# Optimization experiments

Measured on AMD Instinct MI355X. Metric: run time of the kernel, lower is better.

## Reference

```python
import jax, jax.numpy as jnp
import numpy as np

B, S, E, H = 2, 2048, 1024, 16
HD = E // H  # head_dim = 64
NEG = jnp.float32(-1e9)


def setup_inputs() -> dict:
    key = jax.random.key(0)
    k1, k2, k3 = jax.random.split(key, 3)
    x = jax.random.normal(k1, (B, S, E), dtype=jnp.float32)
    w_qkv = jax.random.normal(k2, (E, 3 * E), dtype=jnp.float32) * 0.02
    b_qkv = jnp.zeros((3 * E,), dtype=jnp.float32)
    w_proj = jax.random.normal(k3, (E, E), dtype=jnp.float32) * 0.02
    b_proj = jnp.zeros((E,), dtype=jnp.float32)
    return {"x": x, "w_qkv": w_qkv, "b_qkv": b_qkv, "w_proj": w_proj, "b_proj": b_proj}


def reference(x, w_qkv, b_qkv, w_proj, b_proj):
    # c_attn (GPT2 Conv1D): x @ W + b -> [B,S,3E]
    qkv = x @ w_qkv + b_qkv
    q, k, v = jnp.split(qkv, 3, axis=-1)
    # split heads -> [B,H,S,HD]
    def heads(t):
        return t.reshape(B, S, H, HD).transpose(0, 2, 1, 3)
    q, k, v = heads(q), heads(k), heads(v)
    # scaled QK^T, causal mask, softmax (attn_pdrop=0 so dropout is identity)
    scores = jnp.einsum("bhqd,bhkd->bhqk", q, k) / jnp.sqrt(jnp.float32(HD))
    causal = jnp.tril(jnp.ones((S, S), dtype=bool))
    scores = jnp.where(causal, scores, NEG)
    attn = jax.nn.softmax(scores, axis=-1)
    out = jnp.einsum("bhqk,bhkd->bhqd", attn, v)
    out = out.transpose(0, 2, 1, 3).reshape(B, S, E)
    # c_proj
    return out @ w_proj + b_proj
```

## Files before the change

kernel.cpp:

```cpp
#include <hip/hip_runtime.h>


typedef __bf16 bf16;
typedef __bf16 bf16x4 __attribute__((ext_vector_type(4)));
typedef __bf16 bf16x8 __attribute__((ext_vector_type(8)));
typedef float f32x4 __attribute__((ext_vector_type(4)));

#define GLOBAL_AS(p) ((const __attribute__((address_space(1))) void*)(p))
#define LDS_AS(p) ((__attribute__((address_space(3))) void*)(p))

__device__ __forceinline__ void g2l16(const void* g, void* l) {
  __builtin_amdgcn_global_load_lds(GLOBAL_AS(g), LDS_AS(l), 16, 0, 0);
}

#define QSCL 0.18033688f

__global__ __launch_bounds__(256) void prep_kernel(
    const float* __restrict__ x, const float* __restrict__ wq,
    const float* __restrict__ wp, bf16* __restrict__ Xbf,
    bf16* __restrict__ Wqt, bf16* __restrict__ Wpt) {
  __shared__ float tile[32][33];
  const int t = threadIdx.x;
  const int b = blockIdx.x;
  if (b < 4096) {
    const int i = (b * 256 + t) * 4;
    const float4 v = *(const float4*)(x + i);
    bf16x4 o;
    o.x = (bf16)v.x; o.y = (bf16)v.y; o.z = (bf16)v.z; o.w = (bf16)v.w;
    *(bf16x4*)(Xbf + i) = o;
    return;
  }
  const float* W; bf16* Wt; int C, bx, by;
  if (b < 7168) {
    const int b2 = b - 4096;
    W = wq; Wt = Wqt; C = 3072; bx = b2 % 96; by = b2 / 96;
  } else {
    const int b3 = b - 7168;
    W = wp; Wt = Wpt; C = 1024; bx = b3 & 31; by = b3 >> 5;
  }
  const int c0 = bx * 32, r0 = by * 32;
  const int tx = t & 31, ty = t >> 5;
#pragma unroll
  for (int i = ty; i < 32; i += 8) tile[i][tx] = W[(r0 + i) * C + c0 + tx];
  __syncthreads();
#pragma unroll
  for (int i = ty; i < 32; i += 8)
    Wt[(c0 + i) * 1024 + r0 + tx] = (bf16)tile[tx][i];
}

__global__ __launch_bounds__(256) void gemm_qkv_kernel(
    const bf16* __restrict__ A, const bf16* __restrict__ Bt,
    const float* __restrict__ bias, bf16* __restrict__ Qo,
    bf16* __restrict__ Ko, bf16* __restrict__ Vto) {
  constexpr int K = 1024;
  __shared__ bf16 As[128 * 32];
  __shared__ bf16 Bs[128 * 32];
  const int t = threadIdx.x;
  const int m0 = blockIdx.x * 128;
  const int n0 = blockIdx.y * 128;
  const int wave = t >> 6, lane = t & 63;
  const int wr = (wave >> 1) * 64, wc = (wave & 1) * 64;
  const int lr = lane & 15, lg = lane >> 4;
  f32x4 acc[4][4] = {};
  const bf16* ag = A + (m0 + (t >> 2)) * K + (t & 3) * 8;
  const bf16* bg = Bt + (n0 + (t >> 2)) * K + (t & 3) * 8;
  for (int k0 = 0; k0 < K; k0 += 32) {
    __syncthreads();
    g2l16(ag, &As[t * 8]);
    g2l16(ag + 64 * K, &As[2048 + t * 8]);
    g2l16(bg, &Bs[t * 8]);
    g2l16(bg + 64 * K, &Bs[2048 + t * 8]);
    ag += 32; bg += 32;
    __syncthreads();
    bf16x8 af[4], bfr[4];
#pragma unroll
    for (int i = 0; i < 4; i++)
      af[i] = *(const bf16x8*)&As[(wr + i * 16 + lr) * 32 + lg * 8];
#pragma unroll
    for (int j = 0; j < 4; j++)
      bfr[j] = *(const bf16x8*)&Bs[(wc + j * 16 + lr) * 32 + lg * 8];
#pragma unroll
    for (int i = 0; i < 4; i++)
#pragma unroll
      for (int j = 0; j < 4; j++)
        acc[i][j] = __builtin_amdgcn_mfma_f32_16x16x32_bf16(af[i], bfr[j],
                                                            acc[i][j], 0, 0, 0);
  }
#pragma unroll
  for (int i = 0; i < 4; i++) {
#pragma unroll
    for (int j = 0; j < 4; j++) {
      const int n = n0 + wc + j * 16 + lr;
      const float bv = bias[n];
      if (n0 >= 2048) {
        const int e = n & 1023, h = e >> 6, d = e & 63;
        const int mb = m0 + wr + i * 16 + lg * 4;
        const int b = mb >> 11, s = mb & 2047;
        bf16x4 vv;
#pragma unroll
        for (int r = 0; r < 4; r++) vv[r] = (bf16)(acc[i][j][r] + bv);
        *(bf16x4*)(Vto + ((size_t)((b * 16 + h) * 64 + d)) * 2048 + s) = vv;
      } else {
        const int e = n & 1023, h = e >> 6, d = e & 63;
        const bool isq = (n < 1024);
        bf16* dst = isq ? Qo : Ko;
#pragma unroll
        for (int r = 0; r < 4; r++) {
          const int m = m0 + wr + i * 16 + lg * 4 + r;
          const int b = m >> 11, s = m & 2047;
          const float v = acc[i][j][r] + bv;
          dst[((b * 16 + h) * 2048 + s) * 64 + d] = (bf16)(isq ? v * QSCL : v);
        }
      }
    }
  }
}

__global__ __launch_bounds__(256) void gemm_proj_kernel(
    const bf16* __restrict__ A, const bf16* __restrict__ Bt,
    const float* __restrict__ bias, float* __restrict__ Cf) {
  constexpr int K = 1024, N = 1024;
  __shared__ bf16 As[64 * 32];
  __shared__ bf16 Bs[128 * 32];
  const int t = threadIdx.x;
  const int m0 = blockIdx.x * 64;
  const int n0 = blockIdx.y * 128;
  const int wave = t >> 6, lane = t & 63;
  const int wr = (wave >> 1) * 32, wc = (wave & 1) * 64;
  const int lr = lane & 15, lg = lane >> 4;
  f32x4 acc[2][4] = {};
  const bf16* ag = A + (m0 + (t >> 2)) * K + (t & 3) * 8;
  const bf16* bg = Bt + (n0 + (t >> 2)) * K + (t & 3) * 8;
  for (int k0 = 0; k0 < K; k0 += 32) {
    __syncthreads();
    g2l16(ag, &As[t * 8]);
    g2l16(bg, &Bs[t * 8]);
    g2l16(bg + 64 * K, &Bs[2048 + t * 8]);
    ag += 32; bg += 32;
    __syncthreads();
    bf16x8 af[2], bfr[4];
#pragma unroll
    for (int i = 0; i < 2; i++)
      af[i] = *(const bf16x8*)&As[(wr + i * 16 + lr) * 32 + lg * 8];
#pragma unroll
    for (int j = 0; j < 4; j++)
      bfr[j] = *(const bf16x8*)&Bs[(wc + j * 16 + lr) * 32 + lg * 8];
#pragma unroll
    for (int i = 0; i < 2; i++)
#pragma unroll
      for (int j = 0; j < 4; j++)
        acc[i][j] = __builtin_amdgcn_mfma_f32_16x16x32_bf16(af[i], bfr[j],
                                                            acc[i][j], 0, 0, 0);
  }
#pragma unroll
  for (int i = 0; i < 2; i++) {
#pragma unroll
    for (int j = 0; j < 4; j++) {
      const int n = n0 + wc + j * 16 + lr;
      const float bv = bias[n];
#pragma unroll
      for (int r = 0; r < 4; r++) {
        const int m = m0 + wr + i * 16 + lg * 4 + r;
        Cf[m * N + n] = acc[i][j][r] + bv;
      }
    }
  }
}

__device__ __forceinline__ void stage_kv(const bf16* __restrict__ Kg,
                                         const bf16* __restrict__ Vg, int kb,
                                         bf16* ks, bf16* vs, int t) {
  int u = t, r = u >> 3, c = (u & 7) ^ (r & 7);
  g2l16(Kg + (kb + r) * 64 + c * 8, ks + u * 8);
  g2l16(Vg + r * 2048 + kb + c * 8, vs + u * 8);
  u = 256 + t; r = u >> 3; c = (u & 7) ^ (r & 7);
  g2l16(Kg + (kb + r) * 64 + c * 8, ks + u * 8);
  g2l16(Vg + r * 2048 + kb + c * 8, vs + u * 8);
}

__global__ __launch_bounds__(256, 4) void attn_kernel(
    const bf16* __restrict__ Qb, const bf16* __restrict__ Kb,
    const bf16* __restrict__ Vt, bf16* __restrict__ Obf) {
  __shared__ bf16 Ks[64 * 64];
  __shared__ bf16 Vs[64 * 64];
  __shared__ bf16 Ps[4][16 * 72];
  const int t = threadIdx.x;
  const int w = t >> 6, lane = t & 63;
  const int lr = lane & 15, lg = lane >> 4;
  const int bx = blockIdx.x;
  const int xcd = bx & 7, idx = bx >> 3;
  const int bh = (idx & 3) * 8 + xcd;
  const int strip = 31 - (idx >> 2);
  const int qb = strip * 64 + w * 16;
  const bf16* Qg = Qb + (size_t)bh * 2048 * 64;
  const bf16* Kg = Kb + (size_t)bh * 2048 * 64;
  const bf16* Vg = Vt + (size_t)bh * 64 * 2048;
  bf16x8 bq[2];
#pragma unroll
  for (int h = 0; h < 2; h++)
    bq[h] = *(const bf16x8*)(Qg + (qb + lr) * 64 + h * 32 + lg * 8);
  f32x4 oacc[4] = {};
  float lsum = 0.f;
  bf16* ps = &Ps[w][0];
  const int T = strip + 1;
  for (int ti = 0; ti < T; ++ti) {
    __syncthreads();
    stage_kv(Kg, Vg, ti * 64, Ks, Vs, t);
    __syncthreads();
    const int kb = ti * 64;
    bf16x8 ak[4][2], av[4][2];
#pragma unroll
    for (int j = 0; j < 4; j++) {
      const int row = j * 16 + lr;
#pragma unroll
      for (int h = 0; h < 2; h++)
        ak[j][h] =
            *(const bf16x8*)(Ks + (row * 8 + ((h * 4 + lg) ^ (row & 7))) * 8);
    }
#pragma unroll
    for (int dt = 0; dt < 4; dt++) {
      const int row = dt * 16 + lr;
#pragma unroll
      for (int h = 0; h < 2; h++)
        av[dt][h] =
            *(const bf16x8*)(Vs + (row * 8 + ((h * 4 + lg) ^ (row & 7))) * 8);
    }
    f32x4 sacc[4];
#pragma unroll
    for (int j = 0; j < 4; j++) {
      f32x4 s = {};
      s = __builtin_amdgcn_mfma_f32_16x16x32_bf16(ak[j][0], bq[0], s, 0, 0, 0);
      s = __builtin_amdgcn_mfma_f32_16x16x32_bf16(ak[j][1], bq[1], s, 0, 0, 0);
      sacc[j] = s;
    }
    const bool diag = (kb + 63 > qb);
    bf16x4 pk[4];
#pragma unroll
    for (int j = 0; j < 4; j++)
#pragma unroll
      for (int r = 0; r < 4; r++) {
        float v = sacc[j][r];
        if (diag && (kb + j * 16 + lg * 4 + r > qb + lr)) v = -1e30f;
        const float e = __builtin_amdgcn_exp2f(v);
        lsum += e;
        pk[j][r] = (bf16)e;
      }
    asm volatile("" ::: "memory");
#pragma unroll
    for (int j = 0; j < 4; j++)
      *(bf16x4*)(ps + lr * 72 + j * 16 + lg * 4) = pk[j];
    asm volatile("s_waitcnt lgkmcnt(0)" ::: "memory");
    bf16x8 bp[2];
#pragma unroll
    for (int h = 0; h < 2; h++)
      bp[h] = *(const bf16x8*)(ps + lr * 72 + h * 32 + lg * 8);
#pragma unroll
    for (int dt = 0; dt < 4; dt++) {
      f32x4 o = oacc[dt];
      o = __builtin_amdgcn_mfma_f32_16x16x32_bf16(av[dt][0], bp[0], o, 0, 0, 0);
      o = __builtin_amdgcn_mfma_f32_16x16x32_bf16(av[dt][1], bp[1], o, 0, 0, 0);
      oacc[dt] = o;
    }
  }
  lsum += __shfl_xor(lsum, 16, 64);
  lsum += __shfl_xor(lsum, 32, 64);
  const float inv = 1.0f / lsum;
  const int b = bh >> 4, hh = bh & 15;
  const int q = qb + lr;
  bf16* orow = Obf + ((size_t)(b * 2048 + q)) * 1024 + hh * 64;
#pragma unroll
  for (int dt = 0; dt < 4; dt++) {
    bf16x4 ov;
#pragma unroll
    for (int r = 0; r < 4; r++) ov[r] = (bf16)(oacc[dt][r] * inv);
    *(bf16x4*)(orow + dt * 16 + lg * 4) = ov;
  }
}

extern "C" void kernel_launch(void* const* d_in, const int* in_sizes, int n_in,
                              void* d_out, int out_size, void* d_ws,
                              size_t ws_size, hipStream_t stream) {
  const float* x      = (const float*)d_in[0];
  const float* w_qkv  = (const float*)d_in[1];
  const float* b_qkv  = (const float*)d_in[2];
  const float* w_proj = (const float*)d_in[3];
  const float* b_proj = (const float*)d_in[4];
  float* out = (float*)d_out;

  char* w = (char*)d_ws;
  bf16* Xbf = (bf16*)w;  w += 4096 * 1024 * 2;
  bf16* Wqt = (bf16*)w;  w += 3072 * 1024 * 2;
  bf16* Wpt = (bf16*)w;  w += 1024 * 1024 * 2;
  bf16* Qb  = (bf16*)w;  w += 2 * 16 * 2048 * 64 * 2;
  bf16* Kb  = (bf16*)w;  w += 2 * 16 * 2048 * 64 * 2;
  bf16* Vt  = (bf16*)w;  w += 2 * 16 * 64 * 2048 * 2;
  bf16* Obf = (bf16*)w;  w += 4096 * 1024 * 2;

  prep_kernel<<<8192, 256, 0, stream>>>(x, w_qkv, w_proj, Xbf, Wqt, Wpt);
  gemm_qkv_kernel<<<dim3(32, 24), 256, 0, stream>>>(
      Xbf, Wqt, b_qkv, Qb, Kb, Vt);
  attn_kernel<<<1024, 256, 0, stream>>>(Qb, Kb, Vt, Obf);
  gemm_proj_kernel<<<dim3(64, 8), 256, 0, stream>>>(Obf, Wpt, b_proj, out);
}
```

Baseline: 170.1 us.

## Double K-step to 64 and XOR-swizzle LDS layout in QKV GEMM

The QKV projection GEMM now stages 64-wide K slices per iteration instead of 32, which halves the number of barrier pairs per block. Each 16-byte chunk's column index is XOR-swizzled by its row in LDS, and reads use the same swizzle, to avoid bank conflicts on the fragment loads. This doubles shared memory per block and increases register use for the fragments, which may reduce occupancy.

```diff
diff --git a/kernel.cpp b/kernel.cpp
--- a/kernel.cpp
+++ b/kernel.cpp
@@ -53,8 +53,8 @@
     const float* __restrict__ bias, bf16* __restrict__ Qo,
     bf16* __restrict__ Ko, bf16* __restrict__ Vto) {
   constexpr int K = 1024;
-  __shared__ bf16 As[128 * 32];
-  __shared__ bf16 Bs[128 * 32];
+  __shared__ bf16 As[128 * 64];
+  __shared__ bf16 Bs[128 * 64];
   const int t = threadIdx.x;
   const int m0 = blockIdx.x * 128;
   const int n0 = blockIdx.y * 128;
@@ -62,29 +62,41 @@
   const int wr = (wave >> 1) * 64, wc = (wave & 1) * 64;
   const int lr = lane & 15, lg = lane >> 4;
   f32x4 acc[4][4] = {};
-  const bf16* ag = A + (m0 + (t >> 2)) * K + (t & 3) * 8;
-  const bf16* bg = Bt + (n0 + (t >> 2)) * K + (t & 3) * 8;
-  for (int k0 = 0; k0 < K; k0 += 32) {
-    __syncthreads();
-    g2l16(ag, &As[t * 8]);
-    g2l16(ag + 64 * K, &As[2048 + t * 8]);
-    g2l16(bg, &Bs[t * 8]);
-    g2l16(bg + 64 * K, &Bs[2048 + t * 8]);
-    ag += 32; bg += 32;
-    __syncthreads();
-    bf16x8 af[4], bfr[4];
-#pragma unroll
-    for (int i = 0; i < 4; i++)
-      af[i] = *(const bf16x8*)&As[(wr + i * 16 + lr) * 32 + lg * 8];
-#pragma unroll
-    for (int j = 0; j < 4; j++)
-      bfr[j] = *(const bf16x8*)&Bs[(wc + j * 16 + lr) * 32 + lg * 8];
-#pragma unroll
-    for (int i = 0; i < 4; i++)
-#pragma unroll
-      for (int j = 0; j < 4; j++)
-        acc[i][j] = __builtin_amdgcn_mfma_f32_16x16x32_bf16(af[i], bfr[j],
-                                                            acc[i][j], 0, 0, 0);
+  for (int k0 = 0; k0 < K; k0 += 64) {
+    __syncthreads();
+#pragma unroll
+    for (int p = 0; p < 4; p++) {
+      const int u = p * 256 + t;
+      const int r = u >> 3, c = (u & 7) ^ (r & 7);
+      g2l16(A + (m0 + r) * K + k0 + c * 8, &As[u * 8]);
+      g2l16(Bt + (n0 + r) * K + k0 + c * 8, &Bs[u * 8]);
+    }
+    __syncthreads();
+    bf16x8 af[4][2], bfr[4][2];
+#pragma unroll
+    for (int i = 0; i < 4; i++) {
+      const int row = wr + i * 16 + lr;
+#pragma unroll
+      for (int kk = 0; kk < 2; kk++)
+        af[i][kk] =
+            *(const bf16x8*)&As[(row * 8 + ((kk * 4 + lg) ^ (row & 7))) * 8];
+    }
+#pragma unroll
+    for (int j = 0; j < 4; j++) {
+      const int row = wc + j * 16 + lr;
+#pragma unroll
+      for (int kk = 0; kk < 2; kk++)
+        bfr[j][kk] =
+            *(const bf16x8*)&Bs[(row * 8 + ((kk * 4 + lg) ^ (row & 7))) * 8];
+    }
+#pragma unroll
+    for (int kk = 0; kk < 2; kk++)
+#pragma unroll
+      for (int i = 0; i < 4; i++)
+#pragma unroll
+        for (int j = 0; j < 4; j++)
+          acc[i][j] = __builtin_amdgcn_mfma_f32_16x16x32_bf16(
+              af[i][kk], bfr[j][kk], acc[i][j], 0, 0, 0);
   }
 #pragma unroll
   for (int i = 0; i < 4; i++) {
```

After: 181.8 us. +6.9%, slower.
